# Optimization experiments

Hardware: AMD Instinct MI355X
Metric: run time of the kernel (lower is better)

Reference implementation:

```python
import jax, jax.numpy as jnp
import numpy as np

COMMITMENT_COST = 0.25


def setup_inputs() -> dict:
    key = jax.random.key(0)
    k1, k2 = jax.random.split(key)
    z = jax.random.normal(k1, (8, 256, 64, 64), dtype=jnp.float32)
    # codebook initialized uniform(-1/K, 1/K) in the original; scale a normal sample similarly
    K, D = 4096, 256
    codebook = jax.random.uniform(k2, (K, D), dtype=jnp.float32, minval=-1.0 / K, maxval=1.0 / K)
    return {"z": z, "codebook": codebook}


def reference(z, codebook):
    # z: [B, C, H, W] -> [B, H, W, C]
    B, C, H, W = z.shape
    K, D = codebook.shape  # D == C
    inputs = jnp.transpose(z, (0, 2, 3, 1))          # [B,H,W,D]
    flat = inputs.reshape(-1, D)                     # [N,D]

    d = (jnp.sum(flat ** 2, axis=1, keepdims=True)
         + jnp.sum(codebook ** 2, axis=1)
         - 2.0 * flat @ codebook.T)
    idx = jnp.argmin(d, axis=1)                      # [N]
    encodings = jax.nn.one_hot(idx, K, dtype=flat.dtype)  # [N,K]
    quantized = (encodings @ codebook).reshape(inputs.shape)  # [B,H,W,D]

    e_latent_loss = jnp.mean((jax.lax.stop_gradient(quantized) - inputs) ** 2)
    q_latent_loss = jnp.mean((quantized - jax.lax.stop_gradient(inputs)) ** 2)
    loss = q_latent_loss + COMMITMENT_COST * e_latent_loss

    # straight-through estimator
    quantized = inputs + jax.lax.stop_gradient(quantized - inputs)

    avg_probs = jnp.mean(encodings, axis=0)          # [K]
    perplexity = jnp.exp(-jnp.sum(avg_probs * jnp.log(avg_probs + 1e-10)))

    quantized_out = jnp.transpose(quantized, (0, 3, 1, 2))  # [B,C,H,W]
    return loss, quantized_out, perplexity, encodings, idx[:, None]
```

## Files before the change

### kernel.cpp

```cpp
#include <hip/hip_runtime.h>
#include <math.h>

#define N_ROWS 32768
#define K_CODES 4096
#define D_DIM 256
#define HW 4096
#define CHW 1048576

#define OFF_LOSS  0
#define OFF_QUANT 1ULL
#define OFF_PERP  8388609ULL
#define OFF_ENC   8388610ULL
#define OFF_IDX   142606338ULL

#define WS_RN   0
#define WS_EN   32768
#define WS_KEY  36864
#define WS_CNT  102400
#define WS_LOSS 106496
#define WS_CCNT 106498
#define WS_CNT2 106499
#define WS_THR  106504
#define WS_CAND 139272
#define CAP     1048576
#define WS_CBF  1187848
#define WS_NEED_BYTES ((1187848ULL + 524288ULL) * 4ULL)

#define MARGIN 1.5e-3f
#define LBUF_N 1536

typedef short bf16x8 __attribute__((ext_vector_type(8)));
typedef float f32x4 __attribute__((ext_vector_type(4)));
typedef float f32x2 __attribute__((ext_vector_type(2)));

__device__ __forceinline__ unsigned short f2bf(float f) {
  unsigned u = __float_as_uint(f);
  unsigned r = u + 0x7FFFu + ((u >> 16) & 1u);
  return (unsigned short)(r >> 16);
}

__device__ __forceinline__ void async16(void* lds, const void* g) {
  typedef const __attribute__((address_space(1))) void* gvp;
  typedef __attribute__((address_space(3))) void* lvp;
  __builtin_amdgcn_global_load_lds((gvp)g, (lvp)lds, 16, 0, 0);
}

__device__ __forceinline__ float pairwise_sq_128(const float* __restrict__ p, int stride) {
  float r[8];
#pragma unroll
  for (int j = 0; j < 8; ++j) { float v = p[(size_t)j * stride]; r[j] = v * v; }
#pragma unroll
  for (int g = 1; g < 16; ++g) {
#pragma unroll
    for (int j = 0; j < 8; ++j) { float v = p[(size_t)(g * 8 + j) * stride]; r[j] += v * v; }
  }
  return ((r[0] + r[1]) + (r[2] + r[3])) + ((r[4] + r[5]) + (r[6] + r[7]));
}

__global__ void rownorm_k(const float* __restrict__ z, float* __restrict__ rn) {
  int row = blockIdx.x * 256 + threadIdx.x;
  const float* p = z + (size_t)(row >> 12) * CHW + (row & (HW - 1));
  rn[row] = pairwise_sq_128(p, HW) + pairwise_sq_128(p + (size_t)128 * HW, HW);
}

__global__ void enorm_k(const float* __restrict__ cb, float* __restrict__ en) {
  int k = blockIdx.x * 256 + threadIdx.x;
  const float* p = cb + (size_t)k * D_DIM;
  en[k] = pairwise_sq_128(p, 1) + pairwise_sq_128(p + 128, 1);
}

__global__ void cbbf_k(const float* __restrict__ cb, unsigned short* __restrict__ cbf) {
  int i = (blockIdx.x * 256 + threadIdx.x) * 4;
  float4 v = *(const float4*)(cb + i);
  unsigned d0 = f2bf(v.x) | ((unsigned)f2bf(v.y) << 16);
  unsigned d1 = f2bf(v.z) | ((unsigned)f2bf(v.w) << 16);
  *(int2*)(cbf + i) = make_int2((int)d0, (int)d1);
}

__device__ __forceinline__ void stageB(const unsigned short* __restrict__ cbf,
                                       short* bs, int tile, int ph2, int tid) {
#pragma unroll
  for (int k = 0; k < 4; ++k) {
    int i = tid + k * 256;
    int ks2 = i >> 9, s = i & 511;
    int ct = s >> 6, g = (s >> 4) & 3, m = s & 15;
    const unsigned short* src =
        cbf + (size_t)(tile * 128 + ct * 16 + m) * 256 + ph2 * 64 + ks2 * 32 + g * 8;
    async16(bs + (size_t)i * 8, src);
  }
}

__global__ __launch_bounds__(256, 2) void pass4g_k(
    const float* __restrict__ z, const unsigned short* __restrict__ cbf,
    const float* __restrict__ en, float* __restrict__ rn,
    float* __restrict__ rowmin, float* __restrict__ enc,
    unsigned int* __restrict__ cand, unsigned int* __restrict__ cnt2) {
  __shared__ __align__(16) short ASw[4 * 8 * 64 * 8];
  __shared__ __align__(16) short BS2[2 * 1024 * 8];
  __shared__ unsigned int lbuf[2 * LBUF_N];
  __shared__ float rmf[64];
  __shared__ unsigned int lcnt;

  const int tid = threadIdx.x;
  const int lane = tid & 63;
  const int w = tid >> 6;
  const int row_base = blockIdx.x * 64;
  const float* zb = z + (size_t)(row_base >> 12) * CHW + (row_base & (HW - 1));

  if (tid == 0) lcnt = 0;

  {
    float* pf = (float*)BS2;
    int f4 = tid & 15;
    int r0 = f4 * 4;
    int g16 = tid >> 4;
#pragma unroll
    for (int it = 0; it < 2; ++it) {
      int c_oct = (tid >> 4) + it * 16;
      float4 v[8];
#pragma unroll
      for (int j = 0; j < 8; ++j)
        v[j] = *(const float4*)(zb + (size_t)(c_oct * 8 + j) * HW + r0);
      int s = c_oct >> 2, g = c_oct & 3;
#pragma unroll
      for (int i = 0; i < 4; ++i) {
        int r = r0 + i, rt = r >> 4, m = r & 15;
        int dw[4];
#pragma unroll
        for (int k = 0; k < 4; ++k) {
          unsigned lo = f2bf(((const float*)&v[2 * k])[i]);
          unsigned hi = f2bf(((const float*)&v[2 * k + 1])[i]);
          dw[k] = (int)(lo | (hi << 16));
        }
        *(int4*)&ASw[(((rt * 8 + s) * 64) + g * 16 + m) * 8] =
            make_int4(dw[0], dw[1], dw[2], dw[3]);
#pragma unroll
        for (int j = 0; j < 8; ++j) {
          float x = ((const float*)&v[j])[i];
          pf[(g16 * 64 + r) * 8 + j] = x * x;
        }
      }
      __syncthreads();
      if (tid < 64) {
        float racc[8];
#pragma unroll
        for (int j = 0; j < 8; ++j) racc[j] = pf[(size_t)tid * 8 + j];
        for (int gg = 1; gg < 16; ++gg)
#pragma unroll
          for (int j = 0; j < 8; ++j) racc[j] += pf[(gg * 64 + tid) * 8 + j];
        float h = ((racc[0] + racc[1]) + (racc[2] + racc[3])) +
                  ((racc[4] + racc[5]) + (racc[6] + racc[7]));
        if (it == 0) rmf[tid] = h;
        else rn[row_base + tid] = rmf[tid] + h;
      }
      __syncthreads();
    }
  }

  unsigned rowenc[4];
#pragma unroll
  for (int r = 0; r < 4; ++r)
    rowenc[r] = (unsigned)(row_base + w * 16 + (lane >> 4) * 4 + r) << 12;

  float rmin[4] = {3.4e38f, 3.4e38f, 3.4e38f, 3.4e38f};

  stageB(cbf, BS2, 0, 0, tid);
  int pidx = 0;
  for (int tile = 0; tile < 32; ++tile) {
    float ev[8];
#pragma unroll
    for (int ct = 0; ct < 8; ++ct) ev[ct] = en[tile * 128 + ct * 16 + (lane & 15)];

    f32x4 acc[8];
#pragma unroll
    for (int ct = 0; ct < 8; ++ct) acc[ct] = (f32x4){0.f, 0.f, 0.f, 0.f};

#pragma unroll
    for (int ph2 = 0; ph2 < 4; ++ph2, ++pidx) {
      __syncthreads();
      int nx = pidx + 1;
      if (nx < 128) stageB(cbf, BS2 + (nx & 1) * 8192, nx >> 2, nx & 3, tid);

      const short* bb = BS2 + (pidx & 1) * 8192;
      bf16x8 a0 = *(const bf16x8*)&ASw[((w * 8 + ph2 * 2 + 0) * 64 + lane) * 8];
      bf16x8 a1 = *(const bf16x8*)&ASw[((w * 8 + ph2 * 2 + 1) * 64 + lane) * 8];
      __builtin_amdgcn_s_setprio(1);
#pragma unroll
      for (int ct = 0; ct < 8; ++ct) {
        bf16x8 b0 = *(const bf16x8*)&bb[(ct * 64 + lane) * 8];
        acc[ct] = __builtin_amdgcn_mfma_f32_16x16x32_bf16(a0, b0, acc[ct], 0, 0, 0);
      }
#pragma unroll
      for (int ct = 0; ct < 8; ++ct) {
        bf16x8 b1 = *(const bf16x8*)&bb[(512 + ct * 64 + lane) * 8];
        acc[ct] = __builtin_amdgcn_mfma_f32_16x16x32_bf16(a1, b1, acc[ct], 0, 0, 0);
      }
      __builtin_amdgcn_s_setprio(0);
    }

    {
      f32x2 zz = (f32x2){0.f, 0.f};
      f32x2* dst = (f32x2*)enc + ((size_t)blockIdx.x * 32 + tile) * 4096 + tid;
#pragma unroll
      for (int k = 0; k < 16; ++k)
        __builtin_nontemporal_store(zz, dst + k * 256);
    }

#pragma unroll
    for (int ct = 0; ct < 8; ++ct)
#pragma unroll
      for (int r = 0; r < 4; ++r)
        rmin[r] = fminf(rmin[r], ev[ct] - 2.0f * acc[ct][r]);

    float thr2[4];
#pragma unroll
    for (int r = 0; r < 4; ++r) {
      float v = rmin[r];
      v = fminf(v, __shfl_xor(v, 1));
      v = fminf(v, __shfl_xor(v, 2));
      v = fminf(v, __shfl_xor(v, 4));
      v = fminf(v, __shfl_xor(v, 8));
      thr2[r] = v + MARGIN;
    }

#pragma unroll
    for (int ct = 0; ct < 8; ++ct) {
      unsigned code = (unsigned)(tile * 128 + ct * 16 + (lane & 15));
#pragma unroll
      for (int r = 0; r < 4; ++r) {
        float s = ev[ct] - 2.0f * acc[ct][r];
        if (s <= thr2[r]) {
          unsigned pc = rowenc[r] | code;
          unsigned pos = atomicAdd(&lcnt, 1u);
          if (pos < LBUF_N) {
            lbuf[2 * pos] = pc;
            lbuf[2 * pos + 1] = __float_as_uint(s);
          } else {
            unsigned g = atomicAdd(cnt2, 1u);
            if (g < CAP) cand[g] = pc;
          }
        }
      }
    }
  }

#pragma unroll
  for (int r = 0; r < 4; ++r) {
    float v = rmin[r];
    v = fminf(v, __shfl_xor(v, 1));
    v = fminf(v, __shfl_xor(v, 2));
    v = fminf(v, __shfl_xor(v, 4));
    v = fminf(v, __shfl_xor(v, 8));
    if ((lane & 15) == 0) {
      unsigned row = rowenc[r] >> 12;
      rowmin[row] = v;
      rmf[row & 63] = v;
    }
  }

  __syncthreads();
  unsigned n = lcnt; if (n > LBUF_N) n = LBUF_N;
  for (unsigned i0 = 0; i0 < n; i0 += 256) {
    unsigned i = i0 + tid;
    bool keep = false; unsigned pc = 0;
    if (i < n) {
      pc = lbuf[2 * i];
      float s = __uint_as_float(lbuf[2 * i + 1]);
      keep = (s <= rmf[(pc >> 12) & 63] + MARGIN);
    }
    unsigned long long m = __ballot(keep);
    unsigned wb = 0;
    if ((tid & 63) == 0 && m) wb = atomicAdd(cnt2, (unsigned)__popcll(m));
    wb = __shfl(wb, 0);
    if (keep) {
      unsigned off = (unsigned)__popcll(m & ((1ull << (tid & 63)) - 1ull));
      unsigned g = wb + off;
      if (g < CAP) cand[g] = pc;
    }
  }
}

__global__ void verify_k(const float* __restrict__ z, const float* __restrict__ cb,
                         const float* __restrict__ rn, const float* __restrict__ en,
                         const unsigned int* __restrict__ cand,
                         const unsigned int* __restrict__ cnt,
                         unsigned long long* __restrict__ key) {
  unsigned total = *cnt; if (total > CAP) total = CAP;
  for (unsigned i = blockIdx.x * 256 + threadIdx.x; i < total; i += gridDim.x * 256) {
    unsigned pc = cand[i];
    unsigned row = pc >> 12, code = pc & 4095u;
    const float* x = z + (size_t)(row >> 12) * CHW + (row & (HW - 1));
    const float* e = cb + (size_t)code * D_DIM;
    float acc = 0.0f;
#pragma unroll 8
    for (int c = 0; c < D_DIM; ++c) acc = fmaf(x[(size_t)c * HW], e[c], acc);
    float d = (rn[row] + en[code]) - 2.0f * acc;
    unsigned long long k64 = ((unsigned long long)__float_as_uint(d) << 32) | code;
    atomicMin(&key[row], k64);
  }
}

#define BM 128
#define BN 128
#define BK 32
#define KQ 1024
#define ES_S 36
__global__ __launch_bounds__(256, 3) void argmin_fb(
    const float* __restrict__ z, const float* __restrict__ cb,
    const float* __restrict__ rn, const float* __restrict__ en,
    unsigned long long* __restrict__ key, const unsigned int* __restrict__ guard) {
  if (guard && *guard <= CAP) return;
  __shared__ union {
    struct { float Xs[BK * BM]; float Es[BN * ES_S]; } s;
    struct { float rv[BM * 16]; int ri[BM * 16]; } r;
  } sh;
  const int tid = threadIdx.x;
  const int tx = tid & 15, ty = tid >> 4;
  const int row_base = (blockIdx.x >> 2) * BM;
  const int q = blockIdx.x & 3;
  const float* zb = z + (size_t)(row_base >> 12) * CHW + (row_base & (HW - 1));
  float rnv[8];
#pragma unroll
  for (int i = 0; i < 8; ++i) rnv[i] = rn[row_base + ty * 8 + i];
  float bestV[8]; int bestI[8];
#pragma unroll
  for (int i = 0; i < 8; ++i) { bestV[i] = 3.4e38f; bestI[i] = 0; }
  for (int t0 = q * KQ; t0 < q * KQ + KQ; t0 += BN) {
    float acc[8][8];
#pragma unroll
    for (int i = 0; i < 8; ++i)
#pragma unroll
      for (int j = 0; j < 8; ++j) acc[i][j] = 0.0f;
    for (int kb = 0; kb < D_DIM; kb += BK) {
      __syncthreads();
#pragma unroll
      for (int k = 0; k < 4; ++k) {
        int l4 = tid + k * 256, cl = l4 >> 5, ro = (l4 & 31) << 2;
        *(float4*)&sh.s.Xs[cl * BM + ro] = *(const float4*)(zb + (size_t)(kb + cl) * HW + ro);
      }
#pragma unroll
      for (int k = 0; k < 4; ++k) {
        int l4 = tid + k * 256, kl = l4 >> 3, cq = (l4 & 7) << 2;
        *(float4*)&sh.s.Es[kl * ES_S + cq] =
            *(const float4*)(cb + (size_t)(t0 + kl) * D_DIM + kb + cq);
      }
      __syncthreads();
#pragma unroll
      for (int c4 = 0; c4 < BK / 4; ++c4) {
        float4 ef[8];
#pragma unroll
        for (int j = 0; j < 8; ++j)
          ef[j] = *(const float4*)&sh.s.Es[(tx + 16 * j) * ES_S + c4 * 4];
#pragma unroll
        for (int cc = 0; cc < 4; ++cc) {
          int c = c4 * 4 + cc;
          float4 xa = *(const float4*)&sh.s.Xs[c * BM + ty * 8];
          float4 xb = *(const float4*)&sh.s.Xs[c * BM + ty * 8 + 4];
          float xv[8] = {xa.x, xa.y, xa.z, xa.w, xb.x, xb.y, xb.z, xb.w};
          float evv[8] = {((const float*)&ef[0])[cc], ((const float*)&ef[1])[cc],
                          ((const float*)&ef[2])[cc], ((const float*)&ef[3])[cc],
                          ((const float*)&ef[4])[cc], ((const float*)&ef[5])[cc],
                          ((const float*)&ef[6])[cc], ((const float*)&ef[7])[cc]};
#pragma unroll
          for (int i = 0; i < 8; ++i)
#pragma unroll
            for (int j = 0; j < 8; ++j) acc[i][j] = fmaf(xv[i], evv[j], acc[i][j]);
        }
      }
    }
#pragma unroll
    for (int j = 0; j < 8; ++j) {
      int code = t0 + tx + 16 * j;
      float ev = en[code];
#pragma unroll
      for (int i = 0; i < 8; ++i) {
        float d = (rnv[i] + ev) - 2.0f * acc[i][j];
        if (d < bestV[i]) { bestV[i] = d; bestI[i] = code; }
      }
    }
  }
  __syncthreads();
#pragma unroll
  for (int i = 0; i < 8; ++i) {
    sh.r.rv[(ty * 8 + i) * 16 + tx] = bestV[i];
    sh.r.ri[(ty * 8 + i) * 16 + tx] = bestI[i];
  }
  __syncthreads();
  if (tid < BM) {
    float bv = sh.r.rv[tid * 16]; int bi = sh.r.ri[tid * 16];
    for (int t = 1; t < 16; ++t) {
      float v = sh.r.rv[tid * 16 + t]; int ii = sh.r.ri[tid * 16 + t];
      if (v < bv || (v == bv && ii < bi)) { bv = v; bi = ii; }
    }
    unsigned long long k64 = ((unsigned long long)__float_as_uint(bv) << 32) | (unsigned)bi;
    atomicMin(&key[row_base + tid], k64);
  }
}

__global__ void scatter_k(const unsigned long long* __restrict__ key,
                          unsigned int* __restrict__ counts, float* __restrict__ out) {
  int row = blockIdx.x * 256 + threadIdx.x;
  int bi = (int)(unsigned int)(key[row] & 0xffffffffULL);
  out[OFF_IDX + row] = (float)bi;
  out[OFF_ENC + (size_t)row * K_CODES + bi] = 1.0f;
  atomicAdd(&counts[bi], 1u);
}

__global__ void quant_k(const float* __restrict__ z, const float* __restrict__ cb,
                        const unsigned long long* __restrict__ key, float* __restrict__ out,
                        double* __restrict__ losssum) {
  __shared__ double red[256];
  int bh = blockIdx.x, b = bh >> 6, h = bh & 63;
  int tid = threadIdx.x, w = tid & 63, c0 = tid >> 6;
  int n = (b << 12) + (h << 6) + w;
  int iv = (int)(unsigned int)(key[n] & 0xffffffffULL);
  const float* cbr = cb + (size_t)iv * D_DIM;
  size_t zoff = (size_t)b * CHW + (size_t)(h << 6) + w;
  double s = 0.0;
  for (int c = c0; c < D_DIM; c += 4) {
    float zv = z[zoff + (size_t)c * HW];
    float qv = cbr[c];
    float diff = qv - zv;
    out[OFF_QUANT + zoff + (size_t)c * HW] = zv + diff;
    double dd = (double)qv - (double)zv;
    s += dd * dd;
  }
  red[tid] = s;
  __syncthreads();
  for (int st = 128; st > 0; st >>= 1) {
    if (tid < st) red[tid] += red[tid + st];
    __syncthreads();
  }
  if (tid == 0) atomicAdd(losssum, red[0]);
}

__global__ void final_k(const unsigned int* __restrict__ counts,
                        const double* __restrict__ losssum, float* __restrict__ out) {
  __shared__ double red[256];
  int tid = threadIdx.x;
  double s = 0.0;
  for (int k = tid; k < K_CODES; k += 256) {
    double p = (double)counts[k] / 32768.0;
    s += p * log(p + 1e-10);
  }
  red[tid] = s;
  __syncthreads();
  for (int st = 128; st > 0; st >>= 1) {
    if (tid < st) red[tid] += red[tid + st];
    __syncthreads();
  }
  if (tid == 0) {
    out[OFF_PERP] = (float)exp(-red[0]);
    out[OFF_LOSS] = (float)(1.25 * losssum[0] / 8388608.0);
  }
}

extern "C" void kernel_launch(void* const* d_in, const int* in_sizes, int n_in,
                              void* d_out, int out_size, void* d_ws, size_t ws_size,
                              hipStream_t stream) {
  (void)in_sizes; (void)n_in; (void)out_size;
  const float* z = (const float*)d_in[0];
  const float* cb = (const float*)d_in[1];
  float* out = (float*)d_out;
  float* ws = (float*)d_ws;

  float* rn = ws + WS_RN;
  float* en = ws + WS_EN;
  unsigned long long* key = (unsigned long long*)(ws + WS_KEY);
  unsigned int* counts = (unsigned int*)(ws + WS_CNT);
  double* losssum = (double*)(ws + WS_LOSS);

  hipMemsetAsync(ws + WS_KEY, 0xFF, (size_t)N_ROWS * sizeof(unsigned long long), stream);

  enorm_k<<<K_CODES / 256, 256, 0, stream>>>(cb, en);

  if (ws_size >= WS_NEED_BYTES) {
    unsigned int* cnt2 = (unsigned int*)(ws + WS_CNT2);
    float* rowmin = ws + WS_THR;
    unsigned int* cand = (unsigned int*)(ws + WS_CAND);
    unsigned short* cbf = (unsigned short*)(ws + WS_CBF);
    hipMemsetAsync(ws + WS_CNT, 0, (WS_THR - WS_CNT) * sizeof(float), stream);
    cbbf_k<<<(K_CODES * D_DIM / 4) / 256, 256, 0, stream>>>(cb, cbf);
    pass4g_k<<<N_ROWS / 64, 256, 0, stream>>>(z, cbf, en, rn, rowmin,
                                              out + OFF_ENC, cand, cnt2);
    verify_k<<<1024, 256, 0, stream>>>(z, cb, rn, en, cand, cnt2, key);
    argmin_fb<<<(N_ROWS / BM) * 4, 256, 0, stream>>>(z, cb, rn, en, key, cnt2);
  } else {
    hipMemsetAsync(out + OFF_ENC, 0, (size_t)N_ROWS * K_CODES * sizeof(float), stream);
    rownorm_k<<<N_ROWS / 256, 256, 0, stream>>>(z, rn);
    hipMemsetAsync(ws + WS_CNT, 0, K_CODES * sizeof(unsigned int) + 2 * sizeof(double), stream);
    argmin_fb<<<(N_ROWS / BM) * 4, 256, 0, stream>>>(z, cb, rn, en, key, nullptr);
  }

  scatter_k<<<N_ROWS / 256, 256, 0, stream>>>(key, counts, out);
  quant_k<<<512, 256, 0, stream>>>(z, cb, key, out, losssum);
  final_k<<<1, 256, 0, stream>>>(counts, losssum, out);
}
```

Before: 836.8 us.

## Fuse candidate verification into the distance pass and merge scatter into quantize

Candidates that survive the margin filter are now kept in a block-local LDS buffer and verified in fp32 inside the main bf16 distance kernel, using row norms cached in shared memory. Only overflow goes to the global candidate list, so the standalone verify kernel runs with fewer blocks. The scatter kernel is folded into the quantize kernel, and the global rowmin write is dropped. This cuts global candidate traffic and kernel launches, but adds LDS use (which may lower occupancy) and a strided scalar-load tail at the end of each block.

Result: faster. 760.2 us (-9.2%).

```diff
diff --git a/kernel.cpp b/kernel.cpp
--- a/kernel.cpp
+++ b/kernel.cpp
@@ -28,6 +28,7 @@
 
 #define MARGIN 1.5e-3f
 #define LBUF_N 1536
+#define CBUF_N 640
 
 typedef short bf16x8 __attribute__((ext_vector_type(8)));
 typedef float f32x4 __attribute__((ext_vector_type(4)));
@@ -90,16 +91,19 @@
   }
 }
 
-__global__ __launch_bounds__(256, 2) void pass4g_k(
-    const float* __restrict__ z, const unsigned short* __restrict__ cbf,
+__global__ __launch_bounds__(256, 2) void pass5v_k(
+    const float* __restrict__ z, const float* __restrict__ cb,
+    const unsigned short* __restrict__ cbf,
     const float* __restrict__ en, float* __restrict__ rn,
-    float* __restrict__ rowmin, float* __restrict__ enc,
+    float* __restrict__ enc, unsigned long long* __restrict__ key,
     unsigned int* __restrict__ cand, unsigned int* __restrict__ cnt2) {
   __shared__ __align__(16) short ASw[4 * 8 * 64 * 8];
   __shared__ __align__(16) short BS2[2 * 1024 * 8];
   __shared__ unsigned int lbuf[2 * LBUF_N];
+  __shared__ unsigned int cbuf[CBUF_N];
   __shared__ float rmf[64];
-  __shared__ unsigned int lcnt;
+  __shared__ float rn_s[64];
+  __shared__ unsigned int lcnt, ccnt;
 
   const int tid = threadIdx.x;
   const int lane = tid & 63;
@@ -107,7 +111,7 @@
   const int row_base = blockIdx.x * 64;
   const float* zb = z + (size_t)(row_base >> 12) * CHW + (row_base & (HW - 1));
 
-  if (tid == 0) lcnt = 0;
+  if (tid == 0) { lcnt = 0; ccnt = 0; }
 
   {
     float* pf = (float*)BS2;
@@ -151,7 +155,11 @@
         float h = ((racc[0] + racc[1]) + (racc[2] + racc[3])) +
                   ((racc[4] + racc[5]) + (racc[6] + racc[7]));
         if (it == 0) rmf[tid] = h;
-        else rn[row_base + tid] = rmf[tid] + h;
+        else {
+          float tot = rmf[tid] + h;
+          rn[row_base + tid] = tot;
+          rn_s[tid] = tot;
+        }
       }
       __syncthreads();
     }
@@ -251,11 +259,7 @@
     v = fminf(v, __shfl_xor(v, 2));
     v = fminf(v, __shfl_xor(v, 4));
     v = fminf(v, __shfl_xor(v, 8));
-    if ((lane & 15) == 0) {
-      unsigned row = rowenc[r] >> 12;
-      rowmin[row] = v;
-      rmf[row & 63] = v;
-    }
+    if ((lane & 15) == 0) rmf[(rowenc[r] >> 12) & 63] = v;
   }
 
   __syncthreads();
@@ -270,13 +274,29 @@
     }
     unsigned long long m = __ballot(keep);
     unsigned wb = 0;
-    if ((tid & 63) == 0 && m) wb = atomicAdd(cnt2, (unsigned)__popcll(m));
+    if ((tid & 63) == 0 && m) wb = atomicAdd(&ccnt, (unsigned)__popcll(m));
     wb = __shfl(wb, 0);
     if (keep) {
       unsigned off = (unsigned)__popcll(m & ((1ull << (tid & 63)) - 1ull));
       unsigned g = wb + off;
-      if (g < CAP) cand[g] = pc;
-    }
+      if (g < CBUF_N) cbuf[g] = pc;
+      else { unsigned gg = atomicAdd(cnt2, 1u); if (gg < CAP) cand[gg] = pc; }
+    }
+  }
+
+  __syncthreads();
+  unsigned nv = ccnt; if (nv > CBUF_N) nv = CBUF_N;
+  for (unsigned i = tid; i < nv; i += 256) {
+    unsigned pc = cbuf[i];
+    unsigned row = pc >> 12, code = pc & 4095u;
+    const float* x = z + (size_t)(row >> 12) * CHW + (row & (HW - 1));
+    const float* e = cb + (size_t)code * D_DIM;
+    float acc = 0.0f;
+#pragma unroll 8
+    for (int c = 0; c < D_DIM; ++c) acc = fmaf(x[(size_t)c * HW], e[c], acc);
+    float d = (rn_s[row & 63] + en[code]) - 2.0f * acc;
+    unsigned long long k64 = ((unsigned long long)__float_as_uint(d) << 32) | code;
+    atomicMin(&key[row], k64);
   }
 }
 
@@ -397,23 +417,20 @@
   }
 }
 
-__global__ void scatter_k(const unsigned long long* __restrict__ key,
-                          unsigned int* __restrict__ counts, float* __restrict__ out) {
-  int row = blockIdx.x * 256 + threadIdx.x;
-  int bi = (int)(unsigned int)(key[row] & 0xffffffffULL);
-  out[OFF_IDX + row] = (float)bi;
-  out[OFF_ENC + (size_t)row * K_CODES + bi] = 1.0f;
-  atomicAdd(&counts[bi], 1u);
-}
-
-__global__ void quant_k(const float* __restrict__ z, const float* __restrict__ cb,
-                        const unsigned long long* __restrict__ key, float* __restrict__ out,
-                        double* __restrict__ losssum) {
+__global__ void quant2_k(const float* __restrict__ z, const float* __restrict__ cb,
+                         const unsigned long long* __restrict__ key,
+                         unsigned int* __restrict__ counts, float* __restrict__ out,
+                         double* __restrict__ losssum) {
   __shared__ double red[256];
   int bh = blockIdx.x, b = bh >> 6, h = bh & 63;
   int tid = threadIdx.x, w = tid & 63, c0 = tid >> 6;
   int n = (b << 12) + (h << 6) + w;
   int iv = (int)(unsigned int)(key[n] & 0xffffffffULL);
+  if (c0 == 0) {
+    out[OFF_IDX + n] = (float)iv;
+    out[OFF_ENC + (size_t)n * K_CODES + iv] = 1.0f;
+    atomicAdd(&counts[iv], 1u);
+  }
   const float* cbr = cb + (size_t)iv * D_DIM;
   size_t zoff = (size_t)b * CHW + (size_t)(h << 6) + w;
   double s = 0.0;
@@ -476,14 +493,13 @@
 
   if (ws_size >= WS_NEED_BYTES) {
     unsigned int* cnt2 = (unsigned int*)(ws + WS_CNT2);
-    float* rowmin = ws + WS_THR;
     unsigned int* cand = (unsigned int*)(ws + WS_CAND);
     unsigned short* cbf = (unsigned short*)(ws + WS_CBF);
     hipMemsetAsync(ws + WS_CNT, 0, (WS_THR - WS_CNT) * sizeof(float), stream);
     cbbf_k<<<(K_CODES * D_DIM / 4) / 256, 256, 0, stream>>>(cb, cbf);
-    pass4g_k<<<N_ROWS / 64, 256, 0, stream>>>(z, cbf, en, rn, rowmin,
-                                              out + OFF_ENC, cand, cnt2);
-    verify_k<<<1024, 256, 0, stream>>>(z, cb, rn, en, cand, cnt2, key);
+    pass5v_k<<<N_ROWS / 64, 256, 0, stream>>>(z, cb, cbf, en, rn,
+                                              out + OFF_ENC, key, cand, cnt2);
+    verify_k<<<256, 256, 0, stream>>>(z, cb, rn, en, cand, cnt2, key);
     argmin_fb<<<(N_ROWS / BM) * 4, 256, 0, stream>>>(z, cb, rn, en, key, cnt2);
   } else {
     hipMemsetAsync(out + OFF_ENC, 0, (size_t)N_ROWS * K_CODES * sizeof(float), stream);
@@ -492,7 +508,6 @@
     argmin_fb<<<(N_ROWS / BM) * 4, 256, 0, stream>>>(z, cb, rn, en, key, nullptr);
   }
 
-  scatter_k<<<N_ROWS / 256, 256, 0, stream>>>(key, counts, out);
-  quant_k<<<512, 256, 0, stream>>>(z, cb, key, out, losssum);
+  quant2_k<<<512, 256, 0, stream>>>(z, cb, key, counts, out, losssum);
   final_k<<<1, 256, 0, stream>>>(counts, losssum, out);
 }
```
